# Optimization experiments

Hardware: AMD Instinct MI355X
Metric: run time of the kernel (lower is better)

The kernel has to match this reference:

```python
import jax, jax.numpy as jnp
import numpy as np
import math

B, S, E, H, F = 2, 2048, 1024, 16, 4096
D = E // H
EPS = 1e-5


def _layernorm(x, g, b):
    mu = jnp.mean(x, axis=-1, keepdims=True)
    var = jnp.mean(jnp.square(x - mu), axis=-1, keepdims=True)
    return (x - mu) * jax.lax.rsqrt(var + EPS) * g + b


def _xavier(k, fan_in, fan_out):
    limit = math.sqrt(6.0 / (fan_in + fan_out))
    return jax.random.uniform(k, (fan_in, fan_out), jnp.float32, -limit, limit)


def setup_inputs() -> dict:
    key = jax.random.key(0)
    ks = jax.random.split(key, 8)
    x = jax.random.normal(ks[0], (B, S, E), jnp.float32)
    # causal mask: 1 where attendable, 0 where masked (masked_fill at mask==0)
    mask = jnp.tril(jnp.ones((S, S), jnp.int32))[None, None]  # [1,1,S,S]
    return {
        "x": x,
        "mask": mask,
        "Wq": _xavier(ks[1], E, E), "bq": jnp.zeros((E,), jnp.float32),
        "Wk": _xavier(ks[2], E, E), "bk": jnp.zeros((E,), jnp.float32),
        "Wv": _xavier(ks[3], E, E), "bv": jnp.zeros((E,), jnp.float32),
        "Wo": _xavier(ks[4], E, E), "bo": jnp.zeros((E,), jnp.float32),
        "W1": _xavier(ks[5], E, F), "b1": jnp.zeros((F,), jnp.float32),
        "W2": _xavier(ks[6], F, E), "b2": jnp.zeros((E,), jnp.float32),
        "ln1_g": jnp.ones((E,), jnp.float32), "ln1_b": jnp.zeros((E,), jnp.float32),
        "ln2_g": jnp.ones((E,), jnp.float32), "ln2_b": jnp.zeros((E,), jnp.float32),
    }


def reference(x, mask, Wq, bq, Wk, bk, Wv, bv, Wo, bo, W1, b1, W2, b2,
              ln1_g, ln1_b, ln2_g, ln2_b):
    n = _layernorm(x, ln1_g, ln1_b)
    # project and split heads: [B,S,E] -> [B,H,S,D]
    def heads(w, b):
        return (n @ w + b).reshape(B, S, H, D).transpose(0, 2, 1, 3)
    Q, K, V = heads(Wq, bq), heads(Wk, bk), heads(Wv, bv)
    scores = jnp.einsum('bhsd,bhtd->bhst', Q, K) / math.sqrt(D)  # [B,H,S,S]
    scores = jnp.where(mask == 0, jnp.float32(-1e9), scores)
    attn = jax.nn.softmax(scores, axis=-1)
    ctx = jnp.einsum('bhst,bhtd->bhsd', attn, V)
    ctx = ctx.transpose(0, 2, 1, 3).reshape(B, S, E)
    attn_out = ctx @ Wo + bo
    x = _layernorm(x + attn_out, ln2_g, ln2_b)
    ffn = jax.nn.gelu(x @ W1 + b1, approximate=False) @ W2 + b2
    return x + ffn
```

## Files before the change

### kernel.cpp

```cpp
#include <hip/hip_runtime.h>
#include <cmath>

typedef unsigned short u16;
typedef unsigned int u32;
typedef __bf16 bf16x8 __attribute__((ext_vector_type(8)));
typedef float f32x4 __attribute__((ext_vector_type(4)));

#define SEQ 2048
#define EMB 1024
#define NHEAD 16
#define HDIM 64
#define FFDIM 4096
#define NBATCH 2
#define QKVLD 3072
#define PWS 68

#define QSCALE 0.18033688011112042f

__device__ __forceinline__ u16 f2bf(float f) {
  u32 u = __float_as_uint(f);
  u32 r = u + 0x7fffu + ((u >> 16) & 1u);
  return (u16)(r >> 16);
}

__device__ __forceinline__ float ex2(float x) {
#if __has_builtin(__builtin_amdgcn_exp2f)
  return __builtin_amdgcn_exp2f(x);
#else
  return exp2f(x);
#endif
}

__device__ __forceinline__ float geluf(float x) {
  float u = 0.7978845608028654f * (x + 0.044715f * x * x * x);
  float e = ex2(2.8853900817779268f * u);
  return x - x / (e + 1.0f);
}

__device__ __forceinline__ void gload16(const void* g, void* l) {
  __builtin_amdgcn_global_load_lds(
      (const __attribute__((address_space(1))) unsigned int*)g,
      (__attribute__((address_space(3))) unsigned int*)l, 16, 0, 0);
}

__device__ __forceinline__ u32 lds_addr(const void* p) {
  return (u32)(size_t)(const __attribute__((address_space(3))) void*)p;
}

template <int IMM>
__device__ __forceinline__ bf16x8 dsr16(u32 a) {
  bf16x8 r;
  asm volatile("ds_read_b128 %0, %1 offset:%2" : "=v"(r) : "v"(a), "n"(IMM));
  return r;
}

__global__ __launch_bounds__(256)
void wtrans_kernel(const float* __restrict__ W, u16* __restrict__ WT, int K, int N) {
  __shared__ float tile[32][33];
  int tx = threadIdx.x & 31, ty = threadIdx.x >> 5;
  int n0 = blockIdx.x * 32, k0 = blockIdx.y * 32;
#pragma unroll
  for (int i = 0; i < 32; i += 8)
    tile[ty + i][tx] = W[(size_t)(k0 + ty + i) * N + (n0 + tx)];
  __syncthreads();
#pragma unroll
  for (int i = 0; i < 32; i += 8)
    WT[(size_t)(n0 + ty + i) * K + (k0 + tx)] = f2bf(tile[tx][ty + i]);
}

__global__ __launch_bounds__(256)
void wtrans4_kernel(const float* __restrict__ W0, const float* __restrict__ W1_,
                    const float* __restrict__ W2_, const float* __restrict__ W3,
                    u16* __restrict__ Dqkv, u16* __restrict__ Do) {
  __shared__ float tile[32][33];
  int z = blockIdx.z;
  const float* W = (z == 0) ? W0 : (z == 1) ? W1_ : (z == 2) ? W2_ : W3;
  u16* D = (z < 3) ? (Dqkv + (size_t)z * EMB * EMB) : Do;
  int tx = threadIdx.x & 31, ty = threadIdx.x >> 5;
  int n0 = blockIdx.x * 32, k0 = blockIdx.y * 32;
#pragma unroll
  for (int i = 0; i < 32; i += 8)
    tile[ty + i][tx] = W[(size_t)(k0 + ty + i) * EMB + (n0 + tx)];
  __syncthreads();
#pragma unroll
  for (int i = 0; i < 32; i += 8)
    D[(size_t)(n0 + ty + i) * EMB + (k0 + tx)] = f2bf(tile[tx][ty + i]);
}

__global__ __launch_bounds__(256)
void vtrans_kernel(const u16* __restrict__ QKV, u16* __restrict__ Vt) {
  __shared__ u16 tile[64 * 72];
  int bh = blockIdx.y, b = bh >> 4, h = bh & 15;
  int s0 = blockIdx.x * 64;
  const u16* src = QKV + (size_t)b * SEQ * QKVLD + 2048 + (size_t)h * HDIM;
  int tid = threadIdx.x;
#pragma unroll
  for (int cc = 0; cc < 2; ++cc) {
    int c = tid + cc * 256;
    int s = c >> 3, d0 = (c & 7) * 8;
    uint4 v = *(const uint4*)(src + (size_t)(s0 + s) * QKVLD + d0);
    *(uint4*)(&tile[s * 72 + d0]) = v;
  }
  __syncthreads();
  u16* dst = Vt + (size_t)bh * HDIM * SEQ;
#pragma unroll
  for (int cc = 0; cc < 2; ++cc) {
    int c = tid + cc * 256;
    int d = c >> 3, t0l = (c & 7) * 8;
    union { uint4 u; u16 s[8]; } ou;
#pragma unroll
    for (int j = 0; j < 8; ++j) ou.s[j] = tile[(t0l + j) * 72 + d];
    *(uint4*)(dst + (size_t)d * SEQ + s0 + t0l) = ou.u;
  }
}

__global__ __launch_bounds__(256)
void ln_kernel(const float* __restrict__ in, const float* __restrict__ gamma,
               const float* __restrict__ beta, u16* __restrict__ outb) {
  int w = threadIdx.x >> 6, lane = threadIdx.x & 63;
  int row = blockIdx.x * 4 + w;
  size_t base = (size_t)row * EMB;
  float4 v[4];
  float s = 0.f, q = 0.f;
#pragma unroll
  for (int j = 0; j < 4; ++j) {
    v[j] = *(const float4*)(in + base + j * 256 + lane * 4);
    s += v[j].x + v[j].y + v[j].z + v[j].w;
    q += v[j].x * v[j].x + v[j].y * v[j].y + v[j].z * v[j].z + v[j].w * v[j].w;
  }
#pragma unroll
  for (int off = 1; off < 64; off <<= 1) {
    s += __shfl_xor(s, off);
    q += __shfl_xor(q, off);
  }
  float mean = s * (1.0f / EMB);
  float var = q * (1.0f / EMB) - mean * mean;
  float rstd = rsqrtf(var + 1e-5f);
#pragma unroll
  for (int j = 0; j < 4; ++j) {
    int c = j * 256 + lane * 4;
    float4 g4 = *(const float4*)(gamma + c);
    float4 b4 = *(const float4*)(beta + c);
    ushort4 ob;
    ob.x = f2bf((v[j].x - mean) * rstd * g4.x + b4.x);
    ob.y = f2bf((v[j].y - mean) * rstd * g4.y + b4.y);
    ob.z = f2bf((v[j].z - mean) * rstd * g4.z + b4.z);
    ob.w = f2bf((v[j].w - mean) * rstd * g4.w + b4.w);
    *(ushort4*)(outb + base + c) = ob;
  }
}

__global__ __launch_bounds__(256)
void ln2f_kernel(const float* __restrict__ p, size_t pstride,
                 const float* __restrict__ bias, const float* __restrict__ resid,
                 const float* __restrict__ gamma, const float* __restrict__ beta,
                 u16* __restrict__ outb, float* __restrict__ outf) {
  int w = threadIdx.x >> 6, lane = threadIdx.x & 63;
  int row = blockIdx.x * 4 + w;
  size_t base = (size_t)row * EMB;
  float4 v[4];
  float s = 0.f, q = 0.f;
#pragma unroll
  for (int j = 0; j < 4; ++j) {
    int c = j * 256 + lane * 4;
    float4 a = *(const float4*)(p + base + c);
    float4 b = *(const float4*)(p + pstride + base + c);
    float4 r = *(const float4*)(resid + base + c);
    float4 bb = *(const float4*)(bias + c);
    v[j].x = a.x + b.x + r.x + bb.x;
    v[j].y = a.y + b.y + r.y + bb.y;
    v[j].z = a.z + b.z + r.z + bb.z;
    v[j].w = a.w + b.w + r.w + bb.w;
    s += v[j].x + v[j].y + v[j].z + v[j].w;
    q += v[j].x * v[j].x + v[j].y * v[j].y + v[j].z * v[j].z + v[j].w * v[j].w;
  }
#pragma unroll
  for (int off = 1; off < 64; off <<= 1) {
    s += __shfl_xor(s, off);
    q += __shfl_xor(q, off);
  }
  float mean = s * (1.0f / EMB);
  float var = q * (1.0f / EMB) - mean * mean;
  float rstd = rsqrtf(var + 1e-5f);
#pragma unroll
  for (int j = 0; j < 4; ++j) {
    int c = j * 256 + lane * 4;
    float4 g4 = *(const float4*)(gamma + c);
    float4 b4 = *(const float4*)(beta + c);
    float y0 = (v[j].x - mean) * rstd * g4.x + b4.x;
    float y1 = (v[j].y - mean) * rstd * g4.y + b4.y;
    float y2 = (v[j].z - mean) * rstd * g4.z + b4.z;
    float y3 = (v[j].w - mean) * rstd * g4.w + b4.w;
    ushort4 ob;
    ob.x = f2bf(y0); ob.y = f2bf(y1); ob.z = f2bf(y2); ob.w = f2bf(y3);
    *(ushort4*)(outb + base + c) = ob;
    *(float4*)(outf + base + c) = make_float4(y0, y1, y2, y3);
  }
}

__global__ __launch_bounds__(256)
void reduce2_kernel(const float* __restrict__ p, size_t pstride,
                    const float* __restrict__ bias, const float* __restrict__ resid,
                    float* __restrict__ out, int ncols) {
  size_t i = ((size_t)blockIdx.x * 256 + threadIdx.x) * 4;
  float4 a = *(const float4*)(p + i);
  float4 b = *(const float4*)(p + pstride + i);
  float4 r = *(const float4*)(resid + i);
  int col = (int)(i & (size_t)(ncols - 1));
  float4 bb = *(const float4*)(bias + col);
  float4 o;
  o.x = a.x + b.x + r.x + bb.x;
  o.y = a.y + b.y + r.y + bb.y;
  o.z = a.z + b.z + r.z + bb.z;
  o.w = a.w + b.w + r.w + bb.w;
  *(float4*)(out + i) = o;
}


#define BARM __builtin_amdgcn_s_barrier()
#define VMWS asm volatile("s_waitcnt vmcnt(%0)" ::"n"(4 + RA))
#define VMW0 asm volatile("s_waitcnt vmcnt(0)")
#define NOSTG ((void)0)
#define NOWT ((void)0)

#define STG_A(t, d, kh)                                                       \
  { _Pragma("unroll")                                                         \
    for (int j = 0; j < RA; ++j)                                              \
      gload16(A + (size_t)sgA[j] + kbeg + (t) * 64 + (kh) * 32,               \
              As + ((d) * 2 + (kh)) * ABUF + slA[j]); }

#define STG_B(t, d, kh)                                                       \
  { _Pragma("unroll")                                                         \
    for (int j = 0; j < 2; ++j)                                               \
      gload16(BT + (size_t)sgB[j] + kbeg + (t) * 64 + (kh) * 32,              \
              Bs + ((d) * 2 + (kh)) * 8192 + slB[j]); }

#define PHASE(d, kk, mh, STAGE, WAITC)                                        \
  {                                                                           \
    const u32 bA = bB + ((d) * 2 + (kk)) * 16384;                             \
    const u32 aA = aB + ((d) * 2 + (kk)) * (ABUF * 2);                        \
    if ((mh) == 0) {                                                          \
      bfr[0] = dsr16<0>(bA);                                                  \
      bfr[1] = dsr16<1024>(bA);                                               \
      bfr[2] = dsr16<2048>(bA);                                               \
      bfr[3] = dsr16<3072>(bA);                                               \
    }                                                                         \
    bf16x8 af[MT2];                                                           \
    af[0] = dsr16<(((mh) * MT2 + 0) * 1024)>(aA);                             \
    af[1] = dsr16<(((mh) * MT2 + 1) * 1024)>(aA);                             \
    if constexpr (MT2 > 2) {                                                  \
      af[2] = dsr16<(((mh) * MT2 + 2) * 1024)>(aA);                           \
      af[3] = dsr16<(((mh) * MT2 + 3) * 1024)>(aA);                           \
    }                                                                         \
    STAGE;                                                                    \
    BARM;                                                                     \
    asm volatile("s_waitcnt lgkmcnt(0)");                                     \
    __builtin_amdgcn_sched_barrier(0);                                        \
    __builtin_amdgcn_s_setprio(1);                                            \
    _Pragma("unroll")                                                         \
    for (int mi = 0; mi < MT2; ++mi)                                          \
      _Pragma("unroll")                                                       \
      for (int nt = 0; nt < 4; ++nt)                                          \
        acc[(mh) * MT2 + mi][nt] = __builtin_amdgcn_mfma_f32_16x16x32_bf16(   \
            af[mi], bfr[nt], acc[(mh) * MT2 + mi][nt], 0, 0, 0);              \
    __builtin_amdgcn_s_setprio(0);                                            \
    WAITC;                                                                    \
    BARM;                                                                     \
  }

template <int BM>
__global__ __launch_bounds__(512, 2)
void gemm8(const u16* __restrict__ A, const u16* __restrict__ BT,
           const float* __restrict__ bias, const float* __restrict__ bias2,
           const float* __restrict__ bias3, void* __restrict__ out,
           const float* __restrict__ resid, int M, int N, int K,
           int mode, float scale, int ksplit,
           float* __restrict__ partial, size_t pstride) {
  constexpr int MT = BM / 32;
  constexpr int MT2 = MT / 2;
  constexpr int RA = BM / 128;
  constexpr int ABUF = BM * 32;
  __shared__ __align__(16) u16 As[4 * ABUF];
  __shared__ __align__(16) u16 Bs[4 * 8192];

  int tid = threadIdx.x;
  int lane = tid & 63, w = tid >> 6;
  int wm = w >> 2, wn = w & 3;
  int g = lane >> 4, lr = lane & 15;
  int m0 = blockIdx.y * BM, n0 = blockIdx.x * 256;
  int z = blockIdx.z;
  size_t kbeg = (size_t)z * ksplit;
  int nk = ksplit >> 6, npair = nk >> 1;

  int phys = ((lr & 1) * 4 + g) ^ ((lr >> 1) & 7);
  int aoff = wm * (BM / 2) * 32 + (lr >> 1) * 64 + phys * 8;
  int boff = wn * 2048 + (lr >> 1) * 64 + phys * 8;
  const u32 aB = lds_addr(As) + 2 * aoff;
  const u32 bB = lds_addr(Bs) + 2 * boff;

  int sgA[RA], slA[RA];
#pragma unroll
  for (int j = 0; j < RA; ++j) {
    int c = tid + j * 512;
    int sr = c >> 3, ph = c & 7, l = ph ^ (sr & 7);
    sgA[j] = (m0 + 2 * sr + (l >> 2)) * K + (l & 3) * 8;
    slA[j] = c * 8;
  }
  int sgB[2], slB[2];
#pragma unroll
  for (int j = 0; j < 2; ++j) {
    int c = tid + j * 512;
    int sr = c >> 3, ph = c & 7, l = ph ^ (sr & 7);
    sgB[j] = (n0 + 2 * sr + (l >> 2)) * K + (l & 3) * 8;
    slB[j] = c * 8;
  }

  f32x4 acc[MT][4];
#pragma unroll
  for (int mt = 0; mt < MT; ++mt)
#pragma unroll
    for (int nt = 0; nt < 4; ++nt) {
      acc[mt][nt][0] = 0.f; acc[mt][nt][1] = 0.f;
      acc[mt][nt][2] = 0.f; acc[mt][nt][3] = 0.f;
    }

  bf16x8 bfr[4];

  STG_B(0, 0, 0); STG_A(0, 0, 0); STG_B(0, 0, 1); STG_A(0, 0, 1);
  STG_B(1, 1, 0); STG_A(1, 1, 0); STG_B(1, 1, 1);
  VMWS; BARM;

  for (int it = 0; it < npair - 1; ++it) {
    int t1 = 2 * it + 1, t2 = 2 * it + 2, t3 = 2 * it + 3;
    PHASE(0, 0, 0, STG_A(t1, 1, 1), NOWT)
    PHASE(0, 0, 1, STG_B(t2, 0, 0), NOWT)
    PHASE(0, 1, 0, STG_A(t2, 0, 0), NOWT)
    PHASE(0, 1, 1, STG_B(t2, 0, 1), VMWS)
    PHASE(1, 0, 0, STG_A(t2, 0, 1), NOWT)
    PHASE(1, 0, 1, STG_B(t3, 1, 0), NOWT)
    PHASE(1, 1, 0, STG_A(t3, 1, 0), NOWT)
    PHASE(1, 1, 1, STG_B(t3, 1, 1), VMWS)
  }
  {
    int t1 = nk - 1;
    PHASE(0, 0, 0, STG_A(t1, 1, 1), NOWT)
    PHASE(0, 0, 1, NOSTG, NOWT)
    PHASE(0, 1, 0, NOSTG, NOWT)
    PHASE(0, 1, 1, NOSTG, VMW0)
    PHASE(1, 0, 0, NOSTG, NOWT)
    PHASE(1, 0, 1, NOSTG, NOWT)
    PHASE(1, 1, 0, NOSTG, NOWT)
    PHASE(1, 1, 1, NOSTG, NOWT)
  }

  float* pz = partial + (size_t)z * pstride;
#pragma unroll
  for (int mt = 0; mt < MT; ++mt) {
    int row = m0 + wm * (BM / 2) + mt * 16 + g * 4;
#pragma unroll
    for (int nt = 0; nt < 4; ++nt) {
      int col = n0 + wn * 64 + nt * 16 + lr;
      float bcol;
      if (mode == 3) {
        int which = col >> 10;
        const float* bp = (which == 0) ? bias : (which == 1) ? bias2 : bias3;
        bcol = bp[col & 1023];
      } else if (mode != 4) {
        bcol = bias[col];
      } else {
        bcol = 0.f;
      }
#pragma unroll
      for (int r = 0; r < 4; ++r) {
        float vacc = acc[mt][nt][r] + bcol;
        size_t idx = (size_t)(row + r) * N + col;
        if (mode == 0)      ((u16*)out)[idx] = f2bf(vacc * scale);
        else if (mode == 1) ((u16*)out)[idx] = f2bf(geluf(vacc));
        else if (mode == 2) ((float*)out)[idx] = vacc + resid[idx];
        else if (mode == 3) ((u16*)out)[idx] = f2bf(col < 1024 ? vacc * QSCALE : vacc);
        else                pz[idx] = vacc;
      }
    }
  }
}

__shared__ __align__(16) u16 attn_Kt[64 * 64];
__shared__ __align__(16) u16 attn_VT[64 * 64];
__shared__ __align__(16) u16 attn_Pw[2][4][16 * PWS];

template <int S0>
__device__ __forceinline__ void attn_tile(
    int t0, const int* q0, int w, int g, int lr, const bf16x8& ones,
    bf16x8 (&qf)[2][2], f32x4 (&lacc)[2], f32x4 (&oacc)[2][4]) {
  f32x4 sacc[2][4];
#pragma unroll
  for (int s = S0; s < 2; ++s)
#pragma unroll
    for (int nt = 0; nt < 4; ++nt) {
      sacc[s][nt][0] = 0.f; sacc[s][nt][1] = 0.f;
      sacc[s][nt][2] = 0.f; sacc[s][nt][3] = 0.f;
    }
#pragma unroll
  for (int kk = 0; kk < 2; ++kk)
#pragma unroll
    for (int nt = 0; nt < 4; ++nt) {
      int sw = ((kk * 4 + g) ^ lr) & 7;
      bf16x8 bfr = *(const bf16x8*)(&attn_Kt[(nt * 16 + lr) * 64 + sw * 8]);
      if (S0 == 0)
        sacc[0][nt] = __builtin_amdgcn_mfma_f32_16x16x32_bf16(qf[0][kk], bfr, sacc[0][nt], 0, 0, 0);
      sacc[1][nt] = __builtin_amdgcn_mfma_f32_16x16x32_bf16(qf[1][kk], bfr, sacc[1][nt], 0, 0, 0);
    }

#pragma unroll
  for (int s = S0; s < 2; ++s) {
    bool diag = (t0 == q0[s]);
#pragma unroll
    for (int r = 0; r < 4; ++r) {
#pragma unroll
      for (int nt = 0; nt < 4; ++nt) {
        float pv = ex2(sacc[s][nt][r]);
        if (diag && (nt * 16 + lr > w * 16 + g * 4 + r)) pv = 0.f;
        attn_Pw[s][w][(g * 4 + r) * PWS + nt * 16 + lr] = f2bf(pv);
      }
    }
  }

#pragma unroll
  for (int kk = 0; kk < 2; ++kk) {
    bf16x8 pf0, pf1;
    if (S0 == 0) pf0 = *(const bf16x8*)(&attn_Pw[0][w][lr * PWS + kk * 32 + g * 8]);
    pf1 = *(const bf16x8*)(&attn_Pw[1][w][lr * PWS + kk * 32 + g * 8]);
#pragma unroll
    for (int nt = 0; nt < 4; ++nt) {
      int sw = ((kk * 4 + g) ^ lr) & 7;
      bf16x8 vf = *(const bf16x8*)(&attn_VT[(nt * 16 + lr) * 64 + sw * 8]);
      if (S0 == 0)
        oacc[0][nt] = __builtin_amdgcn_mfma_f32_16x16x32_bf16(pf0, vf, oacc[0][nt], 0, 0, 0);
      oacc[1][nt] = __builtin_amdgcn_mfma_f32_16x16x32_bf16(pf1, vf, oacc[1][nt], 0, 0, 0);
    }
    if (S0 == 0)
      lacc[0] = __builtin_amdgcn_mfma_f32_16x16x32_bf16(pf0, ones, lacc[0], 0, 0, 0);
    lacc[1] = __builtin_amdgcn_mfma_f32_16x16x32_bf16(pf1, ones, lacc[1], 0, 0, 0);
  }
}

__global__ __launch_bounds__(256)
void attn2_kernel(const u16* __restrict__ QKV, const u16* __restrict__ Vt,
                  u16* __restrict__ ctx) {
  int tid = threadIdx.x, lane = tid & 63, w = tid >> 6;
  int g = lane >> 4, lr = lane & 15;
  int bh = blockIdx.y, b = bh >> 4, h = bh & 15;
  int q0[2];
  q0[0] = blockIdx.x * 64;
  q0[1] = (SEQ / 64 - 1 - blockIdx.x) * 64;
  const u16* Qh = QKV + (size_t)b * SEQ * QKVLD + (size_t)h * HDIM;
  const u16* Kh = Qh + 1024;
  const u16* Vth = Vt + (size_t)bh * HDIM * SEQ;

  bf16x8 ones;
#pragma unroll
  for (int j = 0; j < 8; ++j) ones[j] = (__bf16)1.0f;

  bf16x8 qf[2][2];
#pragma unroll
  for (int s = 0; s < 2; ++s)
#pragma unroll
    for (int kk = 0; kk < 2; ++kk)
      qf[s][kk] = *(const bf16x8*)(Qh + (size_t)(q0[s] + w * 16 + lr) * QKVLD + kk * 32 + g * 8);

  f32x4 lacc[2];
  f32x4 oacc[2][4];
#pragma unroll
  for (int s = 0; s < 2; ++s) {
    lacc[s][0] = 0.f; lacc[s][1] = 0.f; lacc[s][2] = 0.f; lacc[s][3] = 0.f;
#pragma unroll
    for (int nt = 0; nt < 4; ++nt) {
      oacc[s][nt][0] = 0.f; oacc[s][nt][1] = 0.f;
      oacc[s][nt][2] = 0.f; oacc[s][nt][3] = 0.f;
    }
  }

  int c1 = tid, c2 = tid + 256;
  int t1 = c1 >> 3, ch1 = (c1 ^ t1) & 7;
  int t2 = c2 >> 3, ch2 = (c2 ^ t2) & 7;
  for (int t0 = 0; t0 <= q0[1]; t0 += 64) {
    __syncthreads();
    gload16(Kh + (size_t)(t0 + t1) * QKVLD + ch1 * 8, attn_Kt + c1 * 8);
    gload16(Kh + (size_t)(t0 + t2) * QKVLD + ch2 * 8, attn_Kt + c2 * 8);
    gload16(Vth + (size_t)t1 * SEQ + t0 + ch1 * 8, attn_VT + c1 * 8);
    gload16(Vth + (size_t)t2 * SEQ + t0 + ch2 * 8, attn_VT + c2 * 8);
    __syncthreads();

    if (t0 <= q0[0])
      attn_tile<0>(t0, q0, w, g, lr, ones, qf, lacc, oacc);
    else
      attn_tile<1>(t0, q0, w, g, lr, ones, qf, lacc, oacc);
  }

#pragma unroll
  for (int s = 0; s < 2; ++s) {
    int srow = q0[s] + w * 16 + g * 4;
    float inv[4];
#pragma unroll
    for (int r = 0; r < 4; ++r) inv[r] = 1.0f / lacc[s][r];
#pragma unroll
    for (int nt = 0; nt < 4; ++nt) {
      int col = h * HDIM + nt * 16 + lr;
#pragma unroll
      for (int r = 0; r < 4; ++r) {
        float o = oacc[s][nt][r] * inv[r];
        ctx[((size_t)b * SEQ + srow + r) * EMB + col] = f2bf(o);
      }
    }
  }
}

extern "C" void kernel_launch(void* const* d_in, const int* in_sizes, int n_in,
                              void* d_out, int out_size, void* d_ws, size_t ws_size,
                              hipStream_t stream) {
  const float* x    = (const float*)d_in[0];
  const float* Wq   = (const float*)d_in[2];
  const float* bq   = (const float*)d_in[3];
  const float* Wk   = (const float*)d_in[4];
  const float* bk   = (const float*)d_in[5];
  const float* Wv   = (const float*)d_in[6];
  const float* bv   = (const float*)d_in[7];
  const float* Wo   = (const float*)d_in[8];
  const float* bo   = (const float*)d_in[9];
  const float* W1   = (const float*)d_in[10];
  const float* b1   = (const float*)d_in[11];
  const float* W2   = (const float*)d_in[12];
  const float* b2   = (const float*)d_in[13];
  const float* ln1g = (const float*)d_in[14];
  const float* ln1b = (const float*)d_in[15];
  const float* ln2g = (const float*)d_in[16];
  const float* ln2b = (const float*)d_in[17];

  char* ws = (char*)d_ws;
  u16* WqkvT = (u16*)(ws + ((size_t)0 << 20));
  u16* WoT   = (u16*)(ws + ((size_t)6 << 20));
  u16* W1T   = (u16*)(ws + ((size_t)8 << 20));
  u16* W2T   = (u16*)(ws + ((size_t)16 << 20));
  u16* xb    = (u16*)(ws + ((size_t)24 << 20));
  u16* QKVb  = (u16*)(ws + ((size_t)32 << 20));
  u16* ctxb  = (u16*)(ws + ((size_t)56 << 20));
  float* x2f = (float*)(ws + ((size_t)48 << 20));
  u16* x2b   = xb;
  u16* VtG   = (u16*)(ws + ((size_t)64 << 20));
  float* pWo = (float*)(ws + ((size_t)64 << 20));
  u16* h1    = (u16*)(ws + ((size_t)64 << 20));
  float* pF2 = (float*)(ws + ((size_t)0 << 20));

  dim3 blk(256);
  dim3 blk512(512);
  const int M = NBATCH * SEQ;

  wtrans4_kernel<<<dim3(32, 32, 4), blk, 0, stream>>>(Wq, Wk, Wv, Wo, WqkvT, WoT);
  wtrans_kernel<<<dim3(128, 32), blk, 0, stream>>>(W1, W1T, EMB, FFDIM);
  wtrans_kernel<<<dim3(32, 128), blk, 0, stream>>>(W2, W2T, FFDIM, EMB);

  ln_kernel<<<M / 4, blk, 0, stream>>>(x, ln1g, ln1b, xb);

  gemm8<256><<<dim3(QKVLD / 256, M / 256), blk512, 0, stream>>>(
      xb, WqkvT, bq, bk, bv, QKVb, nullptr, M, QKVLD, EMB, 3, 1.0f, EMB, nullptr, 0);

  vtrans_kernel<<<dim3(SEQ / 64, NBATCH * NHEAD), blk, 0, stream>>>(QKVb, VtG);

  attn2_kernel<<<dim3(SEQ / 128, NBATCH * NHEAD), blk, 0, stream>>>(QKVb, VtG, ctxb);

  gemm8<128><<<dim3(EMB / 256, M / 128, 2), blk512, 0, stream>>>(
      ctxb, WoT, nullptr, nullptr, nullptr, nullptr, nullptr, M, EMB, EMB, 4, 1.0f,
      EMB / 2, pWo, (size_t)4 << 20);

  ln2f_kernel<<<M / 4, blk, 0, stream>>>(pWo, (size_t)4 << 20, bo, x, ln2g, ln2b,
                                         x2b, x2f);

  gemm8<256><<<dim3(FFDIM / 256, M / 256), blk512, 0, stream>>>(
      x2b, W1T, b1, nullptr, nullptr, h1, nullptr, M, FFDIM, EMB, 1, 1.0f, EMB,
      nullptr, 0);

  gemm8<128><<<dim3(EMB / 256, M / 128, 2), blk512, 0, stream>>>(
      h1, W2T, nullptr, nullptr, nullptr, nullptr, nullptr, M, EMB, FFDIM, 4, 1.0f,
      FFDIM / 2, pF2, (size_t)8 << 20);
  reduce2_kernel<<<M * EMB / 1024, blk, 0, stream>>>(pF2, (size_t)8 << 20, b2, x2f,
                                                     (float*)d_out, EMB);
}
```

Before: 413.4 us.

## Swap QKV and FFN1 GEMMs to simpler tile and pipeline variants

Adds two new GEMM kernels. The QKV projection moves to a simple 128x128-tile, 256-thread kernel with a single-buffered LDS loop, giving more blocks across the device. The FFN1 GEMM moves to a double-buffered per-tile pipeline that issues the whole next tile's loads up front and waits once per tile, in place of the eight-phase staggered schedule. The aim is better occupancy and simpler scheduling for these shapes, at the risk of exposing global-load latency that the old phased pipeline hid.

```diff
diff --git a/kernel.cpp b/kernel.cpp
--- a/kernel.cpp
+++ b/kernel.cpp
@@ -214,6 +214,102 @@
   o.z = a.z + b.z + r.z + bb.z;
   o.w = a.w + b.w + r.w + bb.w;
   *(float4*)(out + i) = o;
+}
+
+__global__ __launch_bounds__(256)
+void gemm_bt(const u16* __restrict__ A, const u16* __restrict__ BT,
+             const float* __restrict__ bias, const float* __restrict__ bias2,
+             const float* __restrict__ bias3, void* __restrict__ out,
+             const float* __restrict__ resid, int M, int N, int K,
+             int mode, float scale, int ksplit,
+             float* __restrict__ partial, size_t pstride) {
+  __shared__ __align__(16) u16 As[128 * 64];
+  __shared__ __align__(16) u16 Bs[128 * 64];
+  int tid = threadIdx.x;
+  int lane = tid & 63, w = tid >> 6;
+  int wm = w >> 1, wn = w & 1;
+  int g = lane >> 4, lr = lane & 15;
+  int m0 = blockIdx.y * 128, n0 = blockIdx.x * 128;
+  int z = blockIdx.z;
+  int kbeg = z * ksplit, kend = kbeg + ksplit;
+
+  f32x4 acc[4][4];
+#pragma unroll
+  for (int mt = 0; mt < 4; ++mt)
+#pragma unroll
+    for (int nt = 0; nt < 4; ++nt) {
+      acc[mt][nt][0] = 0.f; acc[mt][nt][1] = 0.f;
+      acc[mt][nt][2] = 0.f; acc[mt][nt][3] = 0.f;
+    }
+
+  size_t ao[4], bo_[4];
+  int lo[4];
+#pragma unroll
+  for (int cc = 0; cc < 4; ++cc) {
+    int c = tid + cc * 256;
+    int row = c >> 3, slot = c & 7;
+    int gc = slot ^ (row & 7);
+    ao[cc] = (size_t)(m0 + row) * K + gc * 8;
+    bo_[cc] = (size_t)(n0 + row) * K + gc * 8;
+    lo[cc] = c * 8;
+  }
+  int swz[2];
+#pragma unroll
+  for (int kk = 0; kk < 2; ++kk) swz[kk] = ((kk * 4 + g) ^ (lr & 7)) * 8;
+
+  for (int k0 = kbeg; k0 < kend; k0 += 64) {
+    __syncthreads();
+#pragma unroll
+    for (int cc = 0; cc < 4; ++cc) gload16(A + ao[cc] + k0, As + lo[cc]);
+#pragma unroll
+    for (int cc = 0; cc < 4; ++cc) gload16(BT + bo_[cc] + k0, Bs + lo[cc]);
+    __syncthreads();
+#pragma unroll
+    for (int kk = 0; kk < 2; ++kk) {
+      bf16x8 af[4], bfr[4];
+#pragma unroll
+      for (int mt = 0; mt < 4; ++mt)
+        af[mt] = *(const bf16x8*)(As + (wm * 64 + mt * 16 + lr) * 64 + swz[kk]);
+#pragma unroll
+      for (int nt = 0; nt < 4; ++nt)
+        bfr[nt] = *(const bf16x8*)(Bs + (wn * 64 + nt * 16 + lr) * 64 + swz[kk]);
+#pragma unroll
+      for (int mt = 0; mt < 4; ++mt)
+#pragma unroll
+        for (int nt = 0; nt < 4; ++nt)
+          acc[mt][nt] = __builtin_amdgcn_mfma_f32_16x16x32_bf16(af[mt], bfr[nt], acc[mt][nt], 0, 0, 0);
+    }
+  }
+
+  float* pz = partial + (size_t)z * pstride;
+#pragma unroll
+  for (int mt = 0; mt < 4; ++mt) {
+    int row = m0 + wm * 64 + mt * 16 + g * 4;
+#pragma unroll
+    for (int nt = 0; nt < 4; ++nt) {
+      int col = n0 + wn * 64 + nt * 16 + lr;
+      float bcol;
+      if (mode == 3) {
+        int which = col >> 10;
+        const float* bp = (which == 0) ? bias : (which == 1) ? bias2 : bias3;
+        bcol = bp[col & 1023];
+      } else if (mode != 4) {
+        bcol = bias[col];
+      } else {
+        bcol = 0.f;
+      }
+#pragma unroll
+      for (int r = 0; r < 4; ++r) {
+        float vacc = acc[mt][nt][r] + bcol;
+        size_t idx = (size_t)(row + r) * N + col;
+        if (mode == 0)      ((u16*)out)[idx] = f2bf(vacc * scale);
+        else if (mode == 1) ((u16*)out)[idx] = f2bf(geluf(vacc));
+        else if (mode == 2) ((float*)out)[idx] = vacc + resid[idx];
+        else if (mode == 3) ((u16*)out)[idx] = f2bf(col < 1024 ? vacc * QSCALE : vacc);
+        else                pz[idx] = vacc;
+      }
+    }
+  }
 }
 
 
@@ -268,6 +364,123 @@
     BARM;                                                                     \
   }
 
+#define SUB2(d, kk, mh)                                                       \
+  {                                                                           \
+    const u32 bA = bB + ((d) * 2 + (kk)) * 16384;                             \
+    const u32 aA = aB + ((d) * 2 + (kk)) * (ABUF * 2);                        \
+    if ((mh) == 0) {                                                          \
+      bfr[0] = dsr16<0>(bA);                                                  \
+      bfr[1] = dsr16<1024>(bA);                                               \
+      bfr[2] = dsr16<2048>(bA);                                               \
+      bfr[3] = dsr16<3072>(bA);                                               \
+    }                                                                         \
+    bf16x8 af[MT2];                                                           \
+    af[0] = dsr16<(((mh) * MT2 + 0) * 1024)>(aA);                             \
+    af[1] = dsr16<(((mh) * MT2 + 1) * 1024)>(aA);                             \
+    if constexpr (MT2 > 2) {                                                  \
+      af[2] = dsr16<(((mh) * MT2 + 2) * 1024)>(aA);                           \
+      af[3] = dsr16<(((mh) * MT2 + 3) * 1024)>(aA);                           \
+    }                                                                         \
+    asm volatile("s_waitcnt lgkmcnt(0)");                                     \
+    __builtin_amdgcn_sched_barrier(0);                                        \
+    __builtin_amdgcn_s_setprio(1);                                            \
+    _Pragma("unroll")                                                         \
+    for (int mi = 0; mi < MT2; ++mi)                                          \
+      _Pragma("unroll")                                                       \
+      for (int nt = 0; nt < 4; ++nt)                                          \
+        acc[(mh) * MT2 + mi][nt] = __builtin_amdgcn_mfma_f32_16x16x32_bf16(   \
+            af[mi], bfr[nt], acc[(mh) * MT2 + mi][nt], 0, 0, 0);              \
+    __builtin_amdgcn_s_setprio(0);                                            \
+  }
+
+#define TILE2(t, d)                                                           \
+  {                                                                           \
+    if ((t) + 1 < nk) {                                                       \
+      STG_B((t) + 1, (d) ^ 1, 0); STG_A((t) + 1, (d) ^ 1, 0);                 \
+      STG_B((t) + 1, (d) ^ 1, 1); STG_A((t) + 1, (d) ^ 1, 1);                 \
+    }                                                                         \
+    SUB2(d, 0, 0) SUB2(d, 0, 1) SUB2(d, 1, 0) SUB2(d, 1, 1)                   \
+    if ((t) + 1 < nk) { VMW0; }                                               \
+    BARM;                                                                     \
+  }
+
+#define GEMM_EPILOGUE                                                         \
+  float* pz = partial + (size_t)z * pstride;                                  \
+  _Pragma("unroll")                                                           \
+  for (int mt = 0; mt < MT; ++mt) {                                           \
+    int row = m0 + wm * (BM / 2) + mt * 16 + g * 4;                           \
+    _Pragma("unroll")                                                         \
+    for (int nt = 0; nt < 4; ++nt) {                                          \
+      int col = n0 + wn * 64 + nt * 16 + lr;                                  \
+      float bcol;                                                             \
+      if (mode == 3) {                                                        \
+        int which = col >> 10;                                                \
+        const float* bp = (which == 0) ? bias : (which == 1) ? bias2 : bias3; \
+        bcol = bp[col & 1023];                                                \
+      } else if (mode != 4) {                                                 \
+        bcol = bias[col];                                                     \
+      } else {                                                                \
+        bcol = 0.f;                                                           \
+      }                                                                       \
+      _Pragma("unroll")                                                       \
+      for (int r = 0; r < 4; ++r) {                                           \
+        float vacc = acc[mt][nt][r] + bcol;                                   \
+        size_t idx = (size_t)(row + r) * N + col;                             \
+        if (mode == 0)      ((u16*)out)[idx] = f2bf(vacc * scale);            \
+        else if (mode == 1) ((u16*)out)[idx] = f2bf(geluf(vacc));             \
+        else if (mode == 2) ((float*)out)[idx] = vacc + resid[idx];           \
+        else if (mode == 3) ((u16*)out)[idx] = f2bf(col < 1024 ? vacc * QSCALE : vacc); \
+        else                pz[idx] = vacc;                                   \
+      }                                                                       \
+    }                                                                         \
+  }
+
+#define GEMM_PRELUDE                                                          \
+  constexpr int MT = BM / 32;                                                 \
+  constexpr int MT2 = MT / 2;                                                 \
+  constexpr int RA = BM / 128;                                                \
+  constexpr int ABUF = BM * 32;                                               \
+  __shared__ __align__(16) u16 As[4 * ABUF];                                  \
+  __shared__ __align__(16) u16 Bs[4 * 8192];                                  \
+  int tid = threadIdx.x;                                                      \
+  int lane = tid & 63, w = tid >> 6;                                          \
+  int wm = w >> 2, wn = w & 3;                                                \
+  int g = lane >> 4, lr = lane & 15;                                          \
+  int m0 = blockIdx.y * BM, n0 = blockIdx.x * 256;                            \
+  int z = blockIdx.z;                                                         \
+  size_t kbeg = (size_t)z * ksplit;                                           \
+  int nk = ksplit >> 6;                                                       \
+  int phys = ((lr & 1) * 4 + g) ^ ((lr >> 1) & 7);                            \
+  int aoff = wm * (BM / 2) * 32 + (lr >> 1) * 64 + phys * 8;                  \
+  int boff = wn * 2048 + (lr >> 1) * 64 + phys * 8;                           \
+  const u32 aB = lds_addr(As) + 2 * aoff;                                     \
+  const u32 bB = lds_addr(Bs) + 2 * boff;                                     \
+  int sgA[RA], slA[RA];                                                       \
+  _Pragma("unroll")                                                           \
+  for (int j = 0; j < RA; ++j) {                                              \
+    int c = tid + j * 512;                                                    \
+    int sr = c >> 3, ph = c & 7, l = ph ^ (sr & 7);                           \
+    sgA[j] = (m0 + 2 * sr + (l >> 2)) * K + (l & 3) * 8;                      \
+    slA[j] = c * 8;                                                           \
+  }                                                                           \
+  int sgB[2], slB[2];                                                         \
+  _Pragma("unroll")                                                           \
+  for (int j = 0; j < 2; ++j) {                                               \
+    int c = tid + j * 512;                                                    \
+    int sr = c >> 3, ph = c & 7, l = ph ^ (sr & 7);                           \
+    sgB[j] = (n0 + 2 * sr + (l >> 2)) * K + (l & 3) * 8;                      \
+    slB[j] = c * 8;                                                           \
+  }                                                                           \
+  f32x4 acc[MT][4];                                                           \
+  _Pragma("unroll")                                                           \
+  for (int mt = 0; mt < MT; ++mt)                                             \
+    _Pragma("unroll")                                                         \
+    for (int nt = 0; nt < 4; ++nt) {                                          \
+      acc[mt][nt][0] = 0.f; acc[mt][nt][1] = 0.f;                             \
+      acc[mt][nt][2] = 0.f; acc[mt][nt][3] = 0.f;                             \
+    }                                                                         \
+  bf16x8 bfr[4];
+
 template <int BM>
 __global__ __launch_bounds__(512, 2)
 void gemm8(const u16* __restrict__ A, const u16* __restrict__ BT,
@@ -276,55 +489,8 @@
            const float* __restrict__ resid, int M, int N, int K,
            int mode, float scale, int ksplit,
            float* __restrict__ partial, size_t pstride) {
-  constexpr int MT = BM / 32;
-  constexpr int MT2 = MT / 2;
-  constexpr int RA = BM / 128;
-  constexpr int ABUF = BM * 32;
-  __shared__ __align__(16) u16 As[4 * ABUF];
-  __shared__ __align__(16) u16 Bs[4 * 8192];
-
-  int tid = threadIdx.x;
-  int lane = tid & 63, w = tid >> 6;
-  int wm = w >> 2, wn = w & 3;
-  int g = lane >> 4, lr = lane & 15;
-  int m0 = blockIdx.y * BM, n0 = blockIdx.x * 256;
-  int z = blockIdx.z;
-  size_t kbeg = (size_t)z * ksplit;
-  int nk = ksplit >> 6, npair = nk >> 1;
-
-  int phys = ((lr & 1) * 4 + g) ^ ((lr >> 1) & 7);
-  int aoff = wm * (BM / 2) * 32 + (lr >> 1) * 64 + phys * 8;
-  int boff = wn * 2048 + (lr >> 1) * 64 + phys * 8;
-  const u32 aB = lds_addr(As) + 2 * aoff;
-  const u32 bB = lds_addr(Bs) + 2 * boff;
-
-  int sgA[RA], slA[RA];
-#pragma unroll
-  for (int j = 0; j < RA; ++j) {
-    int c = tid + j * 512;
-    int sr = c >> 3, ph = c & 7, l = ph ^ (sr & 7);
-    sgA[j] = (m0 + 2 * sr + (l >> 2)) * K + (l & 3) * 8;
-    slA[j] = c * 8;
-  }
-  int sgB[2], slB[2];
-#pragma unroll
-  for (int j = 0; j < 2; ++j) {
-    int c = tid + j * 512;
-    int sr = c >> 3, ph = c & 7, l = ph ^ (sr & 7);
-    sgB[j] = (n0 + 2 * sr + (l >> 2)) * K + (l & 3) * 8;
-    slB[j] = c * 8;
-  }
-
-  f32x4 acc[MT][4];
-#pragma unroll
-  for (int mt = 0; mt < MT; ++mt)
-#pragma unroll
-    for (int nt = 0; nt < 4; ++nt) {
-      acc[mt][nt][0] = 0.f; acc[mt][nt][1] = 0.f;
-      acc[mt][nt][2] = 0.f; acc[mt][nt][3] = 0.f;
-    }
-
-  bf16x8 bfr[4];
+  GEMM_PRELUDE
+  int npair = nk >> 1;
 
   STG_B(0, 0, 0); STG_A(0, 0, 0); STG_B(0, 0, 1); STG_A(0, 0, 1);
   STG_B(1, 1, 0); STG_A(1, 1, 0); STG_B(1, 1, 1);
@@ -352,36 +518,28 @@
     PHASE(1, 1, 0, NOSTG, NOWT)
     PHASE(1, 1, 1, NOSTG, NOWT)
   }
-
-  float* pz = partial + (size_t)z * pstride;
-#pragma unroll
-  for (int mt = 0; mt < MT; ++mt) {
-    int row = m0 + wm * (BM / 2) + mt * 16 + g * 4;
-#pragma unroll
-    for (int nt = 0; nt < 4; ++nt) {
-      int col = n0 + wn * 64 + nt * 16 + lr;
-      float bcol;
-      if (mode == 3) {
-        int which = col >> 10;
-        const float* bp = (which == 0) ? bias : (which == 1) ? bias2 : bias3;
-        bcol = bp[col & 1023];
-      } else if (mode != 4) {
-        bcol = bias[col];
-      } else {
-        bcol = 0.f;
-      }
-#pragma unroll
-      for (int r = 0; r < 4; ++r) {
-        float vacc = acc[mt][nt][r] + bcol;
-        size_t idx = (size_t)(row + r) * N + col;
-        if (mode == 0)      ((u16*)out)[idx] = f2bf(vacc * scale);
-        else if (mode == 1) ((u16*)out)[idx] = f2bf(geluf(vacc));
-        else if (mode == 2) ((float*)out)[idx] = vacc + resid[idx];
-        else if (mode == 3) ((u16*)out)[idx] = f2bf(col < 1024 ? vacc * QSCALE : vacc);
-        else                pz[idx] = vacc;
-      }
-    }
-  }
+  GEMM_EPILOGUE
+}
+
+template <int BM>
+__global__ __launch_bounds__(512, 2)
+void gemm2p(const u16* __restrict__ A, const u16* __restrict__ BT,
+            const float* __restrict__ bias, const float* __restrict__ bias2,
+            const float* __restrict__ bias3, void* __restrict__ out,
+            const float* __restrict__ resid, int M, int N, int K,
+            int mode, float scale, int ksplit,
+            float* __restrict__ partial, size_t pstride) {
+  GEMM_PRELUDE
+  STG_B(0, 0, 0); STG_A(0, 0, 0); STG_B(0, 0, 1); STG_A(0, 0, 1);
+  VMW0; BARM;
+
+  int npair = nk >> 1;
+  for (int tp = 0; tp < npair; ++tp) {
+    int t0 = 2 * tp, t1 = t0 + 1;
+    TILE2(t0, 0)
+    TILE2(t1, 1)
+  }
+  GEMM_EPILOGUE
 }
 
 __shared__ __align__(16) u16 attn_Kt[64 * 64];
@@ -561,7 +719,7 @@
 
   ln_kernel<<<M / 4, blk, 0, stream>>>(x, ln1g, ln1b, xb);
 
-  gemm8<256><<<dim3(QKVLD / 256, M / 256), blk512, 0, stream>>>(
+  gemm_bt<<<dim3(QKVLD / 128, M / 128), blk, 0, stream>>>(
       xb, WqkvT, bq, bk, bv, QKVb, nullptr, M, QKVLD, EMB, 3, 1.0f, EMB, nullptr, 0);
 
   vtrans_kernel<<<dim3(SEQ / 64, NBATCH * NHEAD), blk, 0, stream>>>(QKVb, VtG);
@@ -575,7 +733,7 @@
   ln2f_kernel<<<M / 4, blk, 0, stream>>>(pWo, (size_t)4 << 20, bo, x, ln2g, ln2b,
                                          x2b, x2f);
 
-  gemm8<256><<<dim3(FFDIM / 256, M / 256), blk512, 0, stream>>>(
+  gemm2p<256><<<dim3(FFDIM / 256, M / 256), blk512, 0, stream>>>(
       x2b, W1T, b1, nullptr, nullptr, h1, nullptr, M, FFDIM, EMB, 1, 1.0f, EMB,
       nullptr, 0);
 
```

Result: no change. 407.4 us (-1.5%).
